# Kernel tuning notes

Measured on AMD Instinct MI355X. Metric: run time of the kernel, lower is better.

Reference implementation:

```python
import jax, jax.numpy as jnp
import numpy as np

E, TOPK = 8, 2
N_EMBD, TEXT_DIM, FULL = 1024, 1024, 1024
BS, SEQ = 8, 512

def setup_inputs() -> dict:
    key = jax.random.key(0)
    ks = jax.random.split(key, 8)
    return {
        "x": jax.random.normal(ks[0], (BS, SEQ, N_EMBD), jnp.float32),
        "dec_embeddings": jax.random.normal(ks[1], (BS, TEXT_DIM), jnp.float32),
        # router is zero-init in the module, but use small random weights so top-k is non-degenerate
        "router_w": jax.random.normal(ks[2], (E, TEXT_DIM), jnp.float32) * 0.02,
        "router_b": jnp.zeros((E,), jnp.float32),
        "w1": jax.random.normal(ks[3], (E, N_EMBD, N_EMBD), jnp.float32) * 0.02,
        "w2": jax.random.normal(ks[4], (E, N_EMBD, FULL), jnp.float32) * 0.02,
        "b1": jnp.zeros((E, 1, N_EMBD), jnp.float32),
        "b2": jnp.zeros((E, 1, FULL), jnp.float32),
    }

def reference(x, dec_embeddings, router_w, router_b, w1, w2, b1, b2):
    bs, seqlen, n_embd = x.shape
    logits = dec_embeddings @ router_w.T + router_b          # (bs, E)
    gate_probs = jax.nn.softmax(logits, axis=-1)
    topk_w, topk_idx = jax.lax.top_k(gate_probs, TOPK)       # (bs, k)
    topk_w = topk_w / jnp.sum(topk_w, axis=-1, keepdims=True)
    # dense all-expert 2-layer MLP (as written in the original)
    hidden = jax.nn.relu(jnp.einsum('bsn,enh->ebsh', x, w1) + b1[:, None])   # (E,bs,S,H)
    out_all = jnp.einsum('ebsh,ehf->ebsf', hidden, w2) + b2[:, None]          # (E,bs,S,F)
    out_b = jnp.transpose(out_all, (1, 0, 2, 3))             # (bs,E,S,F)
    # gather top-k expert outputs per batch item and combine
    sel = jnp.take_along_axis(out_b, topk_idx[:, :, None, None], axis=1)      # (bs,k,S,F)
    final_output = jnp.sum(topk_w[:, :, None, None] * sel, axis=1)            # (bs,S,F)
    combined_mask = jnp.max(jax.nn.one_hot(topk_idx, E, dtype=x.dtype), axis=1)  # (bs,E)
    aux_loss = E * jnp.sum(jnp.mean(gate_probs, axis=0) * jnp.mean(combined_mask, axis=0))
    return final_output, aux_loss, combined_mask, logits
```

## Files before the change

kernel.cpp:

```cpp
#include <hip/hip_runtime.h>
#include <hip/hip_bf16.h>
#include <stdint.h>

#define EXP 8
#define DIM 1024
#define SEQL 512
#define BATCH 8
#define OFF_AUX    4194304
#define OFF_MASK   4194305
#define OFF_LOGITS 4194369

typedef __bf16 bf16_t;
typedef bf16_t bf16x8 __attribute__((ext_vector_type(8)));
typedef bf16_t bf16x4 __attribute__((ext_vector_type(4)));
typedef float  f32x4  __attribute__((ext_vector_type(4)));

typedef __attribute__((address_space(1))) void* as1p;
typedef __attribute__((address_space(3))) void* as3p;

__device__ __forceinline__ void glds16(const void* g, void* l) {
  __builtin_amdgcn_global_load_lds((as1p)(void*)g, (as3p)l, 16, 0, 0);
}

__global__ __launch_bounds__(256) void prep_kernel(
    const float* __restrict__ x, const float* __restrict__ dec,
    const float* __restrict__ rw, const float* __restrict__ rb,
    const float* __restrict__ w1, const float* __restrict__ w2,
    bf16_t* __restrict__ xb, bf16_t* __restrict__ w1t, bf16_t* __restrict__ w2t,
    float* __restrict__ out_aux, float* __restrict__ out_mask,
    float* __restrict__ out_logits, int* __restrict__ idx_ws,
    float* __restrict__ w_ws) {
  __shared__ float tile[64][129];
  __shared__ float part[256];
  __shared__ float lg64[64];
  __shared__ float probs[64];
  __shared__ float msk[64];
  const int bid = blockIdx.x;
  const int t = threadIdx.x;

  if (bid < 2048) {
    const int z = bid >> 7;
    const int rem = bid & 127;
    const int k0 = (rem >> 4) * 128;
    const int n0 = (rem & 15) * 64;
    const float* src = (z < 8) ? (w1 + (size_t)z * DIM * DIM)
                               : (w2 + (size_t)(z - 8) * DIM * DIM);
    bf16_t* dst = (z < 8) ? (w1t + (size_t)z * DIM * DIM)
                          : (w2t + (size_t)(z - 8) * DIM * DIM);
    const int rr = t >> 4, c4 = t & 15;
    float4 v[8];
#pragma unroll
    for (int i = 0; i < 8; ++i)
      v[i] = *(const float4*)(src + (size_t)(k0 + rr + 16 * i) * DIM + n0 + c4 * 4);
#pragma unroll
    for (int i = 0; i < 8; ++i) {
      const int k = rr + 16 * i;
      tile[c4 * 4 + 0][k] = v[i].x;
      tile[c4 * 4 + 1][k] = v[i].y;
      tile[c4 * 4 + 2][k] = v[i].z;
      tile[c4 * 4 + 3][k] = v[i].w;
    }
    __syncthreads();
#pragma unroll
    for (int ii = 0; ii < 4; ++ii) {
      const int n = (t >> 4) + 16 * ii;
      const int c = t & 15;
      bf16x8 o;
#pragma unroll
      for (int wd = 0; wd < 8; ++wd) o[wd] = (bf16_t)tile[n][c * 8 + wd];
      *(bf16x8*)(dst + (size_t)(n0 + n) * DIM + k0 + c * 8) = o;
    }
  } else if (bid < 2048 + 512) {
    const int i0 = (bid - 2048) * 2048 + t;
    float4 v[8];
#pragma unroll
    for (int i = 0; i < 8; ++i) v[i] = ((const float4*)x)[i0 + i * 256];
#pragma unroll
    for (int i = 0; i < 8; ++i) {
      bf16x4 o;
      o[0] = (bf16_t)v[i].x; o[1] = (bf16_t)v[i].y;
      o[2] = (bf16_t)v[i].z; o[3] = (bf16_t)v[i].w;
      ((bf16x4*)xb)[i0 + i * 256] = o;
    }
  } else {
    const int p = t >> 2, seg = t & 3;
    const int b = p >> 3, e = p & 7;
    const float4* dv = (const float4*)(dec + b * DIM + seg * 256);
    const float4* wv = (const float4*)(rw + e * DIM + seg * 256);
    float s = 0.f;
#pragma unroll 8
    for (int i = 0; i < 64; ++i) {
      float4 a = dv[i], c = wv[i];
      s += a.x * c.x + a.y * c.y + a.z * c.z + a.w * c.w;
    }
    part[t] = s;
    __syncthreads();
    if (seg == 0) {
      float l = part[t] + part[t + 1] + part[t + 2] + part[t + 3] + rb[e];
      lg64[p] = l;
      out_logits[p] = l;
    }
    __syncthreads();
    if (t < 8) {
      float l[8];
      float mx = -1e30f;
#pragma unroll
      for (int k = 0; k < 8; ++k) { l[k] = lg64[t * 8 + k]; mx = fmaxf(mx, l[k]); }
      float pe[8];
      float sum = 0.f;
#pragma unroll
      for (int k = 0; k < 8; ++k) { pe[k] = expf(l[k] - mx); sum += pe[k]; }
      float inv = 1.f / sum;
#pragma unroll
      for (int k = 0; k < 8; ++k) { pe[k] *= inv; probs[t * 8 + k] = pe[k]; }
      int i0 = 0;
#pragma unroll
      for (int k = 1; k < 8; ++k) if (pe[k] > pe[i0]) i0 = k;
      int i1 = (i0 == 0) ? 1 : 0;
#pragma unroll
      for (int k = 0; k < 8; ++k) if (k != i0 && pe[k] > pe[i1]) i1 = k;
      float p0 = pe[i0], p1 = pe[i1];
      float invs = 1.f / (p0 + p1);
      idx_ws[t * 2] = i0;
      idx_ws[t * 2 + 1] = i1;
      w_ws[t * 2] = p0 * invs;
      w_ws[t * 2 + 1] = p1 * invs;
#pragma unroll
      for (int k = 0; k < 8; ++k) {
        float m = (k == i0 || k == i1) ? 1.f : 0.f;
        msk[t * 8 + k] = m;
        out_mask[t * 8 + k] = m;
      }
    }
    __syncthreads();
    if (t == 0) {
      float aux = 0.f;
#pragma unroll
      for (int k = 0; k < 8; ++k) {
        float mp = 0.f, mm = 0.f;
#pragma unroll
        for (int bb = 0; bb < 8; ++bb) { mp += probs[bb * 8 + k]; mm += msk[bb * 8 + k]; }
        aux += (mp * 0.125f) * (mm * 0.125f);
      }
      out_aux[0] = 8.f * aux;
    }
  }
}

__device__ __forceinline__ void kloop_64x128(const bf16_t* __restrict__ A,
                                             const bf16_t* __restrict__ Bt,
                                             char* sA, char* sB, int t,
                                             f32x4 acc[2][4]) {
  const int lane = t & 63;
  const int w = t >> 6, wr = w >> 1, wc = w & 1;
  const int m15 = lane & 15, q = lane >> 4;
  const int rl = t >> 2, cp = (t & 3) ^ (rl & 3);
  const bf16_t* ga  = A  + (size_t)rl * DIM + cp * 8;
  const bf16_t* gb0 = Bt + (size_t)rl * DIM + cp * 8;
  const bf16_t* gb1 = gb0 + (size_t)64 * DIM;

  const char* ra[2];
  const char* rb[4];
#pragma unroll
  for (int i = 0; i < 2; ++i) {
    const int r = wr * 32 + i * 16 + m15;
    ra[i] = sA + r * 64 + ((q ^ (r & 3)) * 16);
  }
#pragma unroll
  for (int j = 0; j < 4; ++j) {
    const int n = wc * 64 + j * 16 + m15;
    rb[j] = sB + n * 64 + ((q ^ (n & 3)) * 16);
  }

  glds16(ga,  sA + t * 16);
  glds16(gb0, sB + t * 16);
  glds16(gb1, sB + 4096 + t * 16);

  for (int kt = 0; kt < 32; ++kt) {
    const int cur = kt & 1;
    __syncthreads();
    if (kt < 31) {
      const int nxt = cur ^ 1;
      const int off = (kt + 1) * 32;
      glds16(ga + off,  sA + nxt * 4096 + t * 16);
      glds16(gb0 + off, sB + nxt * 8192 + t * 16);
      glds16(gb1 + off, sB + nxt * 8192 + 4096 + t * 16);
    }
    bf16x8 af[2], bfr[4];
#pragma unroll
    for (int i = 0; i < 2; ++i) af[i] = *(const bf16x8*)(ra[i] + cur * 4096);
#pragma unroll
    for (int j = 0; j < 4; ++j) bfr[j] = *(const bf16x8*)(rb[j] + cur * 8192);
#pragma unroll
    for (int i = 0; i < 2; ++i)
#pragma unroll
      for (int j = 0; j < 4; ++j)
        acc[i][j] = __builtin_amdgcn_mfma_f32_16x16x32_bf16(af[i], bfr[j], acc[i][j], 0, 0, 0);
  }
}

__global__ __launch_bounds__(256) void gemm1_kernel(const bf16_t* __restrict__ xb,
                                                    const bf16_t* __restrict__ w1t,
                                                    const float* __restrict__ b1,
                                                    const int* __restrict__ topk_idx,
                                                    const float* __restrict__ topk_w,
                                                    bf16_t* __restrict__ hidden) {
  __shared__ __align__(16) char smem[24576];
  const int tid = threadIdx.x;
  const int bN = blockIdx.x, bM = blockIdx.y, slot = blockIdx.z;
  const int b = slot >> 1;
  const int e = topk_idx[slot];
  const float gw = topk_w[slot];

  const bf16_t* A  = xb + ((size_t)b * SEQL + bM * 64) * DIM;
  const bf16_t* Bt = w1t + ((size_t)e * DIM + bN * 128) * DIM;

  f32x4 acc[2][4];
#pragma unroll
  for (int i = 0; i < 2; ++i)
#pragma unroll
    for (int j = 0; j < 4; ++j) acc[i][j] = {0.f, 0.f, 0.f, 0.f};

  kloop_64x128(A, Bt, smem, smem + 8192, tid, acc);

  __syncthreads();
  bf16_t* hb = (bf16_t*)smem;
  const int lane = tid & 63, w = tid >> 6;
  const int wr = w >> 1, wc = w & 1;
  const int m15 = lane & 15, q = lane >> 4;
  const float* be = b1 + e * DIM;
#pragma unroll
  for (int i = 0; i < 2; ++i)
#pragma unroll
    for (int j = 0; j < 4; ++j) {
      const int colL = wc * 64 + j * 16 + m15;
      const float bias = be[bN * 128 + colL];
#pragma unroll
      for (int r = 0; r < 4; ++r) {
        const int rowL = wr * 32 + i * 16 + q * 4 + r;
        hb[rowL * 136 + colL] = (bf16_t)(gw * fmaxf(acc[i][j][r] + bias, 0.f));
      }
    }
  __syncthreads();
  bf16_t* H = hidden + (size_t)slot * SEQL * DIM + ((size_t)bM * 64) * DIM + bN * 128;
#pragma unroll
  for (int ii = 0; ii < 4; ++ii) {
    const int r = (tid >> 4) + 16 * ii;
    const int c = tid & 15;
    bf16x8 vv = *(const bf16x8*)(hb + r * 136 + c * 8);
    *(bf16x8*)(H + (size_t)r * DIM + c * 8) = vv;
  }
}

__global__ __launch_bounds__(256) void gemm2_kernel(const bf16_t* __restrict__ hidden,
                                                    const bf16_t* __restrict__ w2t,
                                                    const float* __restrict__ b2,
                                                    const int* __restrict__ topk_idx,
                                                    const float* __restrict__ topk_w,
                                                    float* __restrict__ out) {
  __shared__ __align__(16) char smem[24576];
  const int tid = threadIdx.x;
  const int bN = blockIdx.x, bM = blockIdx.y, b = blockIdx.z;
  const int e0 = topk_idx[b * 2], e1 = topk_idx[b * 2 + 1];
  const float w0 = topk_w[b * 2], w1v = topk_w[b * 2 + 1];

  f32x4 acc[2][4];
#pragma unroll
  for (int i = 0; i < 2; ++i)
#pragma unroll
    for (int j = 0; j < 4; ++j) acc[i][j] = {0.f, 0.f, 0.f, 0.f};

  const bf16_t* A0 = hidden + ((size_t)(b * 2) * SEQL + bM * 64) * DIM;
  const bf16_t* B0 = w2t + ((size_t)e0 * DIM + bN * 128) * DIM;
  kloop_64x128(A0, B0, smem, smem + 8192, tid, acc);

  const bf16_t* A1 = hidden + ((size_t)(b * 2 + 1) * SEQL + bM * 64) * DIM;
  const bf16_t* B1 = w2t + ((size_t)e1 * DIM + bN * 128) * DIM;
  kloop_64x128(A1, B1, smem, smem + 8192, tid, acc);

  __syncthreads();
  float* scr = (float*)smem;
  const int lane = tid & 63, w = tid >> 6;
  const int wr = w >> 1, wc = w & 1;
  const int m15 = lane & 15, q = lane >> 4;
  const float* be0 = b2 + e0 * DIM;
  const float* be1 = b2 + e1 * DIM;
  float bb[4];
#pragma unroll
  for (int j = 0; j < 4; ++j) {
    const int col = bN * 128 + wc * 64 + j * 16 + m15;
    bb[j] = w0 * be0[col] + w1v * be1[col];
  }
  float* O = out + (size_t)b * SEQL * DIM;

#pragma unroll
  for (int half = 0; half < 2; ++half) {
#pragma unroll
    for (int j = 0; j < 4; ++j) {
      const int colL = wc * 64 + j * 16 + m15;
#pragma unroll
      for (int r = 0; r < 4; ++r) {
        const int lrow = wr * 16 + q * 4 + r;
        scr[lrow * 132 + colL] = acc[half][j][r] + bb[j];
      }
    }
    __syncthreads();
#pragma unroll
    for (int ii = 0; ii < 4; ++ii) {
      const int lrow = tid >> 3;
      const int cch = (tid & 7) + 8 * ii;
      const float4 v4 = *(const float4*)(scr + lrow * 132 + cch * 4);
      const int grow = bM * 64 + half * 16 + (lrow < 16 ? lrow : lrow + 16);
      *(float4*)(O + (size_t)grow * DIM + bN * 128 + cch * 4) = v4;
    }
    __syncthreads();
  }
}

extern "C" void kernel_launch(void* const* d_in, const int* in_sizes, int n_in,
                              void* d_out, int out_size, void* d_ws, size_t ws_size,
                              hipStream_t stream) {
  const float* x   = (const float*)d_in[0];
  const float* dec = (const float*)d_in[1];
  const float* rw  = (const float*)d_in[2];
  const float* rb  = (const float*)d_in[3];
  const float* w1  = (const float*)d_in[4];
  const float* w2  = (const float*)d_in[5];
  const float* b1  = (const float*)d_in[6];
  const float* b2  = (const float*)d_in[7];
  float* out = (float*)d_out;

  char* ws = (char*)d_ws;
  bf16_t* xb   = (bf16_t*)(ws);
  bf16_t* w1t  = (bf16_t*)(ws + (8u << 20));
  bf16_t* w2t  = (bf16_t*)(ws + (24u << 20));
  bf16_t* hid  = (bf16_t*)(ws + (40u << 20));
  int*    idxw = (int*)(ws + (56u << 20));
  float*  ww   = (float*)(ws + (56u << 20) + 64);

  hipLaunchKernelGGL(prep_kernel, dim3(2048 + 512 + 1), dim3(256), 0, stream,
                     x, dec, rw, rb, w1, w2, xb, w1t, w2t,
                     out + OFF_AUX, out + OFF_MASK, out + OFF_LOGITS, idxw, ww);
  hipLaunchKernelGGL(gemm1_kernel, dim3(8, 8, 16), dim3(256), 0, stream,
                     xb, w1t, b1, idxw, ww, hid);
  hipLaunchKernelGGL(gemm2_kernel, dim3(8, 8, 8), dim3(256), 0, stream,
                     hid, w2t, b2, idxw, ww, out);
}
```

Measured before the change: 207.6 us.

## Load gemm2 MFMA fragments directly from global and shrink weight-transpose tiles

The weight transpose/convert stage now uses 64x64 tiles with float4 LDS writes and twice as many blocks, which cuts LDS use per block and should raise occupancy. gemm2 drops the LDS-staged k-loop and instead has each wave load bf16 fragments straight from global memory into 16x16x32 MFMAs. It also uses a 128x64 block tile and writes results directly, without an LDS transpose epilogue. This removes LDS traffic and barriers, at the cost of uncoalesced fragment loads that rely on cache, no data reuse across waves, and scattered scalar output stores.

```diff
diff --git a/kernel.cpp b/kernel.cpp
--- a/kernel.cpp
+++ b/kernel.cpp
@@ -30,48 +30,38 @@
     float* __restrict__ out_aux, float* __restrict__ out_mask,
     float* __restrict__ out_logits, int* __restrict__ idx_ws,
     float* __restrict__ w_ws) {
-  __shared__ float tile[64][129];
-  __shared__ float part[256];
-  __shared__ float lg64[64];
-  __shared__ float probs[64];
-  __shared__ float msk[64];
+  __shared__ __align__(16) char smem[64 * 68 * 4];
   const int bid = blockIdx.x;
   const int t = threadIdx.x;
 
-  if (bid < 2048) {
-    const int z = bid >> 7;
-    const int rem = bid & 127;
-    const int k0 = (rem >> 4) * 128;
-    const int n0 = (rem & 15) * 64;
+  if (bid < 4096) {
+    const int z = bid >> 8;
+    const int rem = bid & 255;
+    const int k0 = (rem >> 4) * 64, n0 = (rem & 15) * 64;
     const float* src = (z < 8) ? (w1 + (size_t)z * DIM * DIM)
                                : (w2 + (size_t)(z - 8) * DIM * DIM);
     bf16_t* dst = (z < 8) ? (w1t + (size_t)z * DIM * DIM)
                           : (w2t + (size_t)(z - 8) * DIM * DIM);
-    const int rr = t >> 4, c4 = t & 15;
-    float4 v[8];
-#pragma unroll
-    for (int i = 0; i < 8; ++i)
-      v[i] = *(const float4*)(src + (size_t)(k0 + rr + 16 * i) * DIM + n0 + c4 * 4);
-#pragma unroll
-    for (int i = 0; i < 8; ++i) {
-      const int k = rr + 16 * i;
-      tile[c4 * 4 + 0][k] = v[i].x;
-      tile[c4 * 4 + 1][k] = v[i].y;
-      tile[c4 * 4 + 2][k] = v[i].z;
-      tile[c4 * 4 + 3][k] = v[i].w;
-    }
-    __syncthreads();
-#pragma unroll
-    for (int ii = 0; ii < 4; ++ii) {
-      const int n = (t >> 4) + 16 * ii;
-      const int c = t & 15;
+    float (*tile)[68] = (float (*)[68])smem;
+    const int r = t >> 4, c = t & 15;
+    float4 v[4];
+#pragma unroll
+    for (int i = 0; i < 4; ++i)
+      v[i] = *(const float4*)(src + (size_t)(k0 + r + 16 * i) * DIM + n0 + c * 4);
+#pragma unroll
+    for (int i = 0; i < 4; ++i)
+      *(float4*)&tile[r + 16 * i][c * 4] = v[i];
+    __syncthreads();
+#pragma unroll
+    for (int i2 = 0; i2 < 2; ++i2) {
+      const int n = t & 63, kc = (t >> 6) + 4 * i2;
       bf16x8 o;
 #pragma unroll
-      for (int wd = 0; wd < 8; ++wd) o[wd] = (bf16_t)tile[n][c * 8 + wd];
-      *(bf16x8*)(dst + (size_t)(n0 + n) * DIM + k0 + c * 8) = o;
-    }
-  } else if (bid < 2048 + 512) {
-    const int i0 = (bid - 2048) * 2048 + t;
+      for (int wd = 0; wd < 8; ++wd) o[wd] = (bf16_t)tile[kc * 8 + wd][n];
+      *(bf16x8*)(dst + (size_t)(n0 + n) * DIM + k0 + kc * 8) = o;
+    }
+  } else if (bid < 4096 + 512) {
+    const int i0 = (bid - 4096) * 2048 + t;
     float4 v[8];
 #pragma unroll
     for (int i = 0; i < 8; ++i) v[i] = ((const float4*)x)[i0 + i * 256];
@@ -83,6 +73,10 @@
       ((bf16x4*)xb)[i0 + i * 256] = o;
     }
   } else {
+    float* part  = (float*)smem;
+    float* lg64  = part + 256;
+    float* probs = lg64 + 64;
+    float* msk   = probs + 64;
     const int p = t >> 2, seg = t & 3;
     const int b = p >> 3, e = p & 7;
     const float4* dv = (const float4*)(dec + b * DIM + seg * 256);
@@ -258,62 +252,63 @@
                                                     const int* __restrict__ topk_idx,
                                                     const float* __restrict__ topk_w,
                                                     float* __restrict__ out) {
-  __shared__ __align__(16) char smem[24576];
   const int tid = threadIdx.x;
+  const int lane = tid & 63, w = tid >> 6;
+  const int m15 = lane & 15, q = lane >> 4;
   const int bN = blockIdx.x, bM = blockIdx.y, b = blockIdx.z;
+  const int row0 = bM * 128 + w * 32;
+  const int n0 = bN * 64;
   const int e0 = topk_idx[b * 2], e1 = topk_idx[b * 2 + 1];
+
+  f32x4 acc[2][4];
+#pragma unroll
+  for (int i = 0; i < 2; ++i)
+#pragma unroll
+    for (int j = 0; j < 4; ++j) acc[i][j] = {0.f, 0.f, 0.f, 0.f};
+
+#pragma unroll
+  for (int g = 0; g < 2; ++g) {
+    const int e = (g == 0) ? e0 : e1;
+    const bf16_t* A = hidden + ((size_t)(b * 2 + g) * SEQL + row0) * DIM;
+    const bf16_t* B = w2t + ((size_t)e * DIM + n0) * DIM;
+    const bf16_t* pa[2];
+    const bf16_t* pb[4];
+#pragma unroll
+    for (int i = 0; i < 2; ++i) pa[i] = A + (size_t)(i * 16 + m15) * DIM + q * 8;
+#pragma unroll
+    for (int j = 0; j < 4; ++j) pb[j] = B + (size_t)(j * 16 + m15) * DIM + q * 8;
+
+#pragma unroll 4
+    for (int kt = 0; kt < 32; ++kt) {
+      const int off = kt * 32;
+      bf16x8 af[2], bfr[4];
+#pragma unroll
+      for (int i = 0; i < 2; ++i) af[i] = *(const bf16x8*)(pa[i] + off);
+#pragma unroll
+      for (int j = 0; j < 4; ++j) bfr[j] = *(const bf16x8*)(pb[j] + off);
+#pragma unroll
+      for (int i = 0; i < 2; ++i)
+#pragma unroll
+        for (int j = 0; j < 4; ++j)
+          acc[i][j] = __builtin_amdgcn_mfma_f32_16x16x32_bf16(af[i], bfr[j], acc[i][j], 0, 0, 0);
+    }
+  }
+
   const float w0 = topk_w[b * 2], w1v = topk_w[b * 2 + 1];
-
-  f32x4 acc[2][4];
-#pragma unroll
-  for (int i = 0; i < 2; ++i)
-#pragma unroll
-    for (int j = 0; j < 4; ++j) acc[i][j] = {0.f, 0.f, 0.f, 0.f};
-
-  const bf16_t* A0 = hidden + ((size_t)(b * 2) * SEQL + bM * 64) * DIM;
-  const bf16_t* B0 = w2t + ((size_t)e0 * DIM + bN * 128) * DIM;
-  kloop_64x128(A0, B0, smem, smem + 8192, tid, acc);
-
-  const bf16_t* A1 = hidden + ((size_t)(b * 2 + 1) * SEQL + bM * 64) * DIM;
-  const bf16_t* B1 = w2t + ((size_t)e1 * DIM + bN * 128) * DIM;
-  kloop_64x128(A1, B1, smem, smem + 8192, tid, acc);
-
-  __syncthreads();
-  float* scr = (float*)smem;
-  const int lane = tid & 63, w = tid >> 6;
-  const int wr = w >> 1, wc = w & 1;
-  const int m15 = lane & 15, q = lane >> 4;
   const float* be0 = b2 + e0 * DIM;
   const float* be1 = b2 + e1 * DIM;
-  float bb[4];
+  float* O = out + (size_t)b * SEQL * DIM;
 #pragma unroll
   for (int j = 0; j < 4; ++j) {
-    const int col = bN * 128 + wc * 64 + j * 16 + m15;
-    bb[j] = w0 * be0[col] + w1v * be1[col];
-  }
-  float* O = out + (size_t)b * SEQL * DIM;
-
-#pragma unroll
-  for (int half = 0; half < 2; ++half) {
-#pragma unroll
-    for (int j = 0; j < 4; ++j) {
-      const int colL = wc * 64 + j * 16 + m15;
-#pragma unroll
-      for (int r = 0; r < 4; ++r) {
-        const int lrow = wr * 16 + q * 4 + r;
-        scr[lrow * 132 + colL] = acc[half][j][r] + bb[j];
-      }
-    }
-    __syncthreads();
-#pragma unroll
-    for (int ii = 0; ii < 4; ++ii) {
-      const int lrow = tid >> 3;
-      const int cch = (tid & 7) + 8 * ii;
-      const float4 v4 = *(const float4*)(scr + lrow * 132 + cch * 4);
-      const int grow = bM * 64 + half * 16 + (lrow < 16 ? lrow : lrow + 16);
-      *(float4*)(O + (size_t)grow * DIM + bN * 128 + cch * 4) = v4;
-    }
-    __syncthreads();
+    const int col = n0 + j * 16 + m15;
+    const float bb = w0 * be0[col] + w1v * be1[col];
+#pragma unroll
+    for (int i = 0; i < 2; ++i) {
+      const int row = row0 + i * 16 + q * 4;
+#pragma unroll
+      for (int r = 0; r < 4; ++r)
+        O[(size_t)(row + r) * DIM + col] = acc[i][j][r] + bb;
+    }
   }
 }
 
@@ -338,11 +333,11 @@
   int*    idxw = (int*)(ws + (56u << 20));
   float*  ww   = (float*)(ws + (56u << 20) + 64);
 
-  hipLaunchKernelGGL(prep_kernel, dim3(2048 + 512 + 1), dim3(256), 0, stream,
+  hipLaunchKernelGGL(prep_kernel, dim3(4096 + 512 + 1), dim3(256), 0, stream,
                      x, dec, rw, rb, w1, w2, xb, w1t, w2t,
                      out + OFF_AUX, out + OFF_MASK, out + OFF_LOGITS, idxw, ww);
   hipLaunchKernelGGL(gemm1_kernel, dim3(8, 8, 16), dim3(256), 0, stream,
                      xb, w1t, b1, idxw, ww, hid);
-  hipLaunchKernelGGL(gemm2_kernel, dim3(8, 8, 8), dim3(256), 0, stream,
+  hipLaunchKernelGGL(gemm2_kernel, dim3(16, 4, 8), dim3(256), 0, stream,
                      hid, w2t, b2, idxw, ww, out);
 }
```

New measurement: 264.7 us. +27.5%, slower.
